# Kernel optimization log

Measured on AMD Instinct MI355X. Metric: run time of the kernel, lower is better.

Reference implementation:

```python
import jax, jax.numpy as jnp
import numpy as np

L, N, I, H = 512, 64, 1024, 1024


def setup_inputs() -> dict:
    key = jax.random.key(0)
    ks = jax.random.split(key, 7)
    s = 0.05
    return {
        "x": jax.random.normal(ks[0], (L, N, I), dtype=jnp.float32),
        "h0": jnp.zeros((N, H), dtype=jnp.float32),
        "c0": jnp.zeros((N, H), dtype=jnp.float32),
        "W_ih": jax.random.normal(ks[1], (4 * H, I), dtype=jnp.float32) * s,
        "W_hh": jax.random.normal(ks[2], (4 * H, H), dtype=jnp.float32) * s,
        "b_ih": jax.random.normal(ks[3], (4 * H,), dtype=jnp.float32) * s,
        "b_hh": jax.random.normal(ks[4], (4 * H,), dtype=jnp.float32) * s,
        "W_out": jax.random.normal(ks[5], (I, H), dtype=jnp.float32) * s,
        "b_out": jax.random.normal(ks[6], (I,), dtype=jnp.float32) * s,
    }


def reference(x, h0, c0, W_ih, W_hh, b_ih, b_hh, W_out, b_out):
    # PyTorch LSTMCell gate order: input, forget, cell(g), output
    b = b_ih + b_hh  # fuse the two bias adds

    def step(carry, xt):
        h, c = carry
        z = xt @ W_ih.T + h @ W_hh.T + b  # [N, 4H]
        i, f, g, o = jnp.split(z, 4, axis=1)
        c = jax.nn.sigmoid(f) * c + jax.nn.sigmoid(i) * jnp.tanh(g)
        h = jax.nn.sigmoid(o) * jnp.tanh(c)
        return (h, c), None

    (h, c), _ = jax.lax.scan(step, (h0, c0), x)
    y = h @ W_out.T + b_out  # [N, I]
    return (y, h, c)
```

## Files before the change

### kernel.cpp

```cpp
#include <hip/hip_runtime.h>
#include <hip/hip_bf16.h>


#define L_STEPS 512
#define NB 64
#define HID 1024
#define GRID_LSTM 128

typedef __bf16 bf16x8 __attribute__((ext_vector_type(8)));
typedef __bf16 bf16x4 __attribute__((ext_vector_type(4)));
typedef __bf16 bf16x2 __attribute__((ext_vector_type(2)));
typedef float  f32x4  __attribute__((ext_vector_type(4)));
typedef float  f32x2  __attribute__((ext_vector_type(2)));
typedef unsigned u32x4 __attribute__((ext_vector_type(4)));

__device__ __forceinline__ float sigmoid_f(float x) {
    return 1.f / (1.f + __expf(-x));
}
__device__ __forceinline__ float tanh_f(float x) {
    return 1.f - 2.f / (1.f + __expf(2.f * x));
}

__global__ void convert_kernel(const float* __restrict__ x, const float* __restrict__ h0,
                               __bf16* __restrict__ xbf, __bf16* __restrict__ hbf,
                               unsigned* __restrict__ bar) {
    unsigned u = blockIdx.x * 256u + threadIdx.x;
    if (u < 512u) bar[u] = 0u;
    const int row = u & 63;
    const int cg  = (u >> 6) & 127;
    if (u < 8192u) {
        const float* s = h0 + (size_t)row * HID + cg * 8;
        f32x4 a = *(const f32x4*)s, b = *(const f32x4*)(s + 4);
        bf16x8 o;
        o[0]=(__bf16)a[0]; o[1]=(__bf16)a[1]; o[2]=(__bf16)a[2]; o[3]=(__bf16)a[3];
        o[4]=(__bf16)b[0]; o[5]=(__bf16)b[1]; o[6]=(__bf16)b[2]; o[7]=(__bf16)b[3];
        ((bf16x8*)hbf)[u] = o;
    }
    const int t = u >> 13;
    const float* s = x + ((size_t)t * NB + row) * HID + cg * 8;
    f32x4 a = *(const f32x4*)s, b = *(const f32x4*)(s + 4);
    bf16x8 o;
    o[0]=(__bf16)a[0]; o[1]=(__bf16)a[1]; o[2]=(__bf16)a[2]; o[3]=(__bf16)a[3];
    o[4]=(__bf16)b[0]; o[5]=(__bf16)b[1]; o[6]=(__bf16)b[2]; o[7]=(__bf16)b[3];
    ((bf16x8*)xbf)[u] = o;
}

__device__ __forceinline__ void mfma_x(const __bf16* __restrict__ act,
                                       const bf16x8 (&wfr)[2][8],
                                       f32x4 (&acc)[2][4]) {
    #pragma unroll
    for (int kk = 0; kk < 8; ++kk) {
        bf16x8 bfr[4];
        #pragma unroll
        for (int nt = 0; nt < 4; ++nt)
            bfr[nt] = *(const bf16x8*)(act + kk * 2048 + nt * 128);
        #pragma unroll
        for (int mt = 0; mt < 2; ++mt)
            #pragma unroll
            for (int nt = 0; nt < 4; ++nt)
                acc[mt][nt] = __builtin_amdgcn_mfma_f32_16x16x32_bf16(
                    wfr[mt][kk], bfr[nt], acc[mt][nt], 0, 0, 0);
    }
}

template <bool RING>
__global__ __launch_bounds__(256, 1) void lstm_kernel(
    const float* __restrict__ c0,
    const float* __restrict__ W_ih, const float* __restrict__ W_hh,
    const float* __restrict__ b_ih, const float* __restrict__ b_hh,
    const __bf16* __restrict__ xbf,
    __bf16* hbuf,
    unsigned* bar,
    float* __restrict__ out)
{
    const int tid  = threadIdx.x;
    const int lane = tid & 63;
    const int w    = tid >> 6;
    const int quad = lane >> 4;
    const int l15  = lane & 15;
    const int hbase = blockIdx.x * 8;

    __shared__ float red[4][64][44];

    bf16x8 wfx[2][8], wfh[2][8];
    #pragma unroll
    for (int mt = 0; mt < 2; ++mt) {
        const int n    = mt * 16 + l15;
        const int grow = (n >> 3) * HID + hbase + (n & 7);
        #pragma unroll
        for (int kk = 0; kk < 8; ++kk) {
            const int kcol = w * 256 + kk * 32 + quad * 8;
            {
                const float* src = W_ih + (size_t)grow * 1024 + kcol;
                f32x4 a = *(const f32x4*)src;
                f32x4 b = *(const f32x4*)(src + 4);
                bf16x8 f;
                f[0]=(__bf16)a[0]; f[1]=(__bf16)a[1]; f[2]=(__bf16)a[2]; f[3]=(__bf16)a[3];
                f[4]=(__bf16)b[0]; f[5]=(__bf16)b[1]; f[6]=(__bf16)b[2]; f[7]=(__bf16)b[3];
                wfx[mt][kk] = f;
            }
            {
                const float* src = W_hh + (size_t)grow * 1024 + kcol;
                f32x4 a = *(const f32x4*)src;
                f32x4 b = *(const f32x4*)(src + 4);
                bf16x8 f;
                f[0]=(__bf16)a[0]; f[1]=(__bf16)a[1]; f[2]=(__bf16)a[2]; f[3]=(__bf16)a[3];
                f[4]=(__bf16)b[0]; f[5]=(__bf16)b[1]; f[6]=(__bf16)b[2]; f[7]=(__bf16)b[3];
                wfh[mt][kk] = f;
            }
        }
    }

    const int p0 = tid * 2;
    const int cb = p0 >> 3;
    const int cu = p0 & 7;
    float c0v = c0[cb * HID + hbase + cu];
    float c1v = c0[cb * HID + hbase + cu + 1];

    float bias0[4], bias1[4];
    #pragma unroll
    for (int gate = 0; gate < 4; ++gate) {
        int gr = gate * HID + hbase + cu;
        bias0[gate] = b_ih[gr] + b_hh[gr];
        bias1[gate] = b_ih[gr + 1] + b_hh[gr + 1];
    }

    const int lane_off = (32 * w + quad) * 512 + l15 * 8;
    const int hstore_off = blockIdx.x * 512 + cb * 8 + cu;

    f32x4 acc[2][4];
    #pragma unroll
    for (int mt = 0; mt < 2; ++mt)
        #pragma unroll
        for (int nt = 0; nt < 4; ++nt) { f32x4 z = {0.f,0.f,0.f,0.f}; acc[mt][nt] = z; }
    mfma_x(xbf + lane_off, wfx, acc);

    const int pf0 = 128 * w + lane;
    const int pf1 = 128 * w + 64 + lane;

    for (int t = 0; t < L_STEPS; ++t) {
        for (;;) {
            unsigned f0 = __hip_atomic_load(&bar[pf0], __ATOMIC_RELAXED,
                                            __HIP_MEMORY_SCOPE_AGENT);
            unsigned f1 = __hip_atomic_load(&bar[pf1], __ATOMIC_RELAXED,
                                            __HIP_MEMORY_SCOPE_AGENT);
            if (__all((f0 >= (unsigned)t) && (f1 >= (unsigned)t))) break;
            __builtin_amdgcn_s_sleep(1);
        }

        u32x4 hb[8][4];
        const __bf16* hb_base = hbuf
            + (size_t)(RING ? t : (t & 1)) * (NB * HID) + lane_off;
        #pragma unroll
        for (int kk = 0; kk < 8; ++kk)
            #pragma unroll
            for (int nt = 0; nt < 4; ++nt) {
                const __bf16* p = hb_base + kk * 2048 + nt * 128;
                if constexpr (RING)
                    asm volatile("global_load_dwordx4 %0, %1, off"
                                 : "=v"(hb[kk][nt]) : "v"(p));
                else
                    asm volatile("global_load_dwordx4 %0, %1, off sc1"
                                 : "=v"(hb[kk][nt]) : "v"(p));
            }
        asm volatile("s_waitcnt vmcnt(16)"
            : "+v"(hb[0][0]), "+v"(hb[0][1]), "+v"(hb[0][2]), "+v"(hb[0][3]),
              "+v"(hb[1][0]), "+v"(hb[1][1]), "+v"(hb[1][2]), "+v"(hb[1][3]),
              "+v"(hb[2][0]), "+v"(hb[2][1]), "+v"(hb[2][2]), "+v"(hb[2][3]),
              "+v"(hb[3][0]), "+v"(hb[3][1]), "+v"(hb[3][2]), "+v"(hb[3][3]));
        #pragma unroll
        for (int kk = 0; kk < 4; ++kk)
            #pragma unroll
            for (int mt = 0; mt < 2; ++mt)
                #pragma unroll
                for (int nt = 0; nt < 4; ++nt)
                    acc[mt][nt] = __builtin_amdgcn_mfma_f32_16x16x32_bf16(
                        wfh[mt][kk], __builtin_bit_cast(bf16x8, hb[kk][nt]),
                        acc[mt][nt], 0, 0, 0);
        asm volatile("s_waitcnt vmcnt(0)"
            : "+v"(hb[4][0]), "+v"(hb[4][1]), "+v"(hb[4][2]), "+v"(hb[4][3]),
              "+v"(hb[5][0]), "+v"(hb[5][1]), "+v"(hb[5][2]), "+v"(hb[5][3]),
              "+v"(hb[6][0]), "+v"(hb[6][1]), "+v"(hb[6][2]), "+v"(hb[6][3]),
              "+v"(hb[7][0]), "+v"(hb[7][1]), "+v"(hb[7][2]), "+v"(hb[7][3]));
        #pragma unroll
        for (int kk = 4; kk < 8; ++kk)
            #pragma unroll
            for (int mt = 0; mt < 2; ++mt)
                #pragma unroll
                for (int nt = 0; nt < 4; ++nt)
                    acc[mt][nt] = __builtin_amdgcn_mfma_f32_16x16x32_bf16(
                        wfh[mt][kk], __builtin_bit_cast(bf16x8, hb[kk][nt]),
                        acc[mt][nt], 0, 0, 0);

        __syncthreads();

        #pragma unroll
        for (int mt = 0; mt < 2; ++mt)
            #pragma unroll
            for (int nt = 0; nt < 4; ++nt) {
                const int row0 = mt * 16 + quad * 4;
                const int col  = nt * 16 + l15;
                *(f32x4*)&red[w][col][row0] = acc[mt][nt];
            }
        __syncthreads();

        float h0v, h1v;
        {
            float z0[4], z1[4];
            #pragma unroll
            for (int gate = 0; gate < 4; ++gate) {
                const int row = gate * 8 + cu;
                f32x2 s0 = *(const f32x2*)&red[0][cb][row];
                f32x2 s1 = *(const f32x2*)&red[1][cb][row];
                f32x2 s2 = *(const f32x2*)&red[2][cb][row];
                f32x2 s3 = *(const f32x2*)&red[3][cb][row];
                z0[gate] = s0[0] + s1[0] + s2[0] + s3[0] + bias0[gate];
                z1[gate] = s0[1] + s1[1] + s2[1] + s3[1] + bias1[gate];
            }
            float ig = sigmoid_f(z0[0]), fg = sigmoid_f(z0[1]);
            float gg = tanh_f(z0[2]),    og = sigmoid_f(z0[3]);
            c0v = fg * c0v + ig * gg;
            h0v = og * tanh_f(c0v);
            ig = sigmoid_f(z1[0]); fg = sigmoid_f(z1[1]);
            gg = tanh_f(z1[2]);    og = sigmoid_f(z1[3]);
            c1v = fg * c1v + ig * gg;
            h1v = og * tanh_f(c1v);
        }

        {
            bf16x2 hv; hv[0] = (__bf16)h0v; hv[1] = (__bf16)h1v;
            unsigned hbits = __builtin_bit_cast(unsigned, hv);
            const __bf16* dst = hbuf
                + (size_t)(RING ? (t + 1) : ((t + 1) & 1)) * (NB * HID) + hstore_off;
            asm volatile("global_store_dword %0, %1, off sc1"
                         :: "v"(dst), "v"(hbits) : "memory");
        }
        if (t == L_STEPS - 1) {
            const int idx = cb * HID + hbase + cu;
            out[65536 + idx]      = h0v;
            out[65536 + idx + 1]  = h1v;
            out[131072 + idx]     = c0v;
            out[131072 + idx + 1] = c1v;
        }
        asm volatile("s_waitcnt vmcnt(0)" ::: "memory");
        if (lane == 0)
            __hip_atomic_store(&bar[blockIdx.x * 4 + w], (unsigned)(t + 1),
                               __ATOMIC_RELAXED, __HIP_MEMORY_SCOPE_AGENT);

        #pragma unroll
        for (int mt = 0; mt < 2; ++mt)
            #pragma unroll
            for (int nt = 0; nt < 4; ++nt) { f32x4 z = {0.f,0.f,0.f,0.f}; acc[mt][nt] = z; }
        if (t < L_STEPS - 1)
            mfma_x(xbf + (size_t)(t + 1) * (NB * HID) + lane_off, wfx, acc);
    }
}

__global__ void out_kernel(const float* __restrict__ base, const float* __restrict__ Wout,
                           const float* __restrict__ bout, float* __restrict__ y)
{
    const int wv   = (int)((blockIdx.x * 256u + threadIdx.x) >> 6);
    const int lane = threadIdx.x & 63;
    const int b = wv >> 10;
    const int i = wv & 1023;
    const f32x4* hp = (const f32x4*)(base + 65536 + b * HID);
    const f32x4* wp = (const f32x4*)(Wout + (size_t)i * HID);
    float acc = 0.f;
    #pragma unroll
    for (int q = 0; q < 4; ++q) {
        f32x4 hv = hp[q * 64 + lane];
        f32x4 wvv = wp[q * 64 + lane];
        acc += hv[0]*wvv[0] + hv[1]*wvv[1] + hv[2]*wvv[2] + hv[3]*wvv[3];
    }
    #pragma unroll
    for (int off = 32; off > 0; off >>= 1) acc += __shfl_down(acc, off);
    if (lane == 0) y[b * HID + i] = acc + bout[i];
}

extern "C" void kernel_launch(void* const* d_in, const int* in_sizes, int n_in,
                              void* d_out, int out_size, void* d_ws, size_t ws_size,
                              hipStream_t stream)
{
    const float* x    = (const float*)d_in[0];
    const float* h0   = (const float*)d_in[1];
    const float* c0   = (const float*)d_in[2];
    const float* W_ih = (const float*)d_in[3];
    const float* W_hh = (const float*)d_in[4];
    const float* b_ih = (const float*)d_in[5];
    const float* b_hh = (const float*)d_in[6];
    const float* Wout = (const float*)d_in[7];
    const float* bout = (const float*)d_in[8];
    float* out = (float*)d_out;

    const size_t XBF_B  = 67108864;
    const size_t RING_B = 513ull * 131072;
    const size_t need_ring = XBF_B + RING_B + 2048;
    const bool ring = ws_size >= need_ring;

    char* ws = (char*)d_ws;
    __bf16* xbf   = (__bf16*)(ws);
    __bf16* hbuf  = (__bf16*)(ws + XBF_B);
    unsigned* bar = (unsigned*)(ws + XBF_B + (ring ? RING_B : 262144));

    convert_kernel<<<16384, 256, 0, stream>>>(x, h0, xbf, hbuf, bar);
    if (ring)
        lstm_kernel<true><<<GRID_LSTM, 256, 0, stream>>>(c0, W_ih, W_hh, b_ih, b_hh,
                                                         xbf, hbuf, bar, out);
    else
        lstm_kernel<false><<<GRID_LSTM, 256, 0, stream>>>(c0, W_ih, W_hh, b_ih, b_hh,
                                                          xbf, hbuf, bar, out);
    out_kernel<<<16384, 256, 0, stream>>>(out, Wout, bout, out);
}
```

Baseline: 2.918 ms.

## Replace flag barrier with poison-value polling on ring buffer hidden state

In ring mode, the per-wave flag barrier is removed. Every ring slot after the first is prefilled with a poison bit pattern during conversion, and consumers read h directly, reloading any chunk that still contains the poison value. This removes the flag store, the vmcnt drain before it and the separate flag polling from the per-step critical path. The trade-off is a correctness risk: a legitimate bf16 pair equal to the poison pattern would spin forever. The prefill also adds extra write traffic in the convert kernel.

```diff
diff --git a/kernel.cpp b/kernel.cpp
--- a/kernel.cpp
+++ b/kernel.cpp
@@ -6,6 +6,7 @@
 #define NB 64
 #define HID 1024
 #define GRID_LSTM 128
+#define PZN 0xAAAAAAAAu
 
 typedef __bf16 bf16x8 __attribute__((ext_vector_type(8)));
 typedef __bf16 bf16x4 __attribute__((ext_vector_type(4)));
@@ -23,7 +24,7 @@
 
 __global__ void convert_kernel(const float* __restrict__ x, const float* __restrict__ h0,
                                __bf16* __restrict__ xbf, __bf16* __restrict__ hbf,
-                               unsigned* __restrict__ bar) {
+                               unsigned* __restrict__ bar, int ring) {
     unsigned u = blockIdx.x * 256u + threadIdx.x;
     if (u < 512u) bar[u] = 0u;
     const int row = u & 63;
@@ -36,6 +37,10 @@
         o[4]=(__bf16)b[0]; o[5]=(__bf16)b[1]; o[6]=(__bf16)b[2]; o[7]=(__bf16)b[3];
         ((bf16x8*)hbf)[u] = o;
     }
+    if (ring) {
+        u32x4 P = {PZN, PZN, PZN, PZN};
+        ((u32x4*)(hbf + NB * HID))[u] = P;
+    }
     const int t = u >> 13;
     const float* s = x + ((size_t)t * NB + row) * HID + cg * 8;
     f32x4 a = *(const f32x4*)s, b = *(const f32x4*)(s + 4);
@@ -62,6 +67,41 @@
                     wfr[mt][kk], bfr[nt], acc[mt][nt], 0, 0, 0);
     }
 }
+
+template <int K0>
+__device__ __forceinline__ unsigned pmask16(const u32x4 (&hb)[8][4]) {
+    unsigned bad = 0u;
+    #pragma unroll
+    for (int kk = K0; kk < K0 + 4; ++kk)
+        #pragma unroll
+        for (int nt = 0; nt < 4; ++nt) {
+            const u32x4 v = hb[kk][nt];
+            bad |= (unsigned)(v[0] == PZN);
+            bad |= (unsigned)(v[1] == PZN);
+            bad |= (unsigned)(v[2] == PZN);
+            bad |= (unsigned)(v[3] == PZN);
+        }
+    return bad;
+}
+
+template <int K0>
+__device__ __forceinline__ void reload16(u32x4 (&hb)[8][4], const __bf16* hb_base) {
+    #pragma unroll
+    for (int kk = K0; kk < K0 + 4; ++kk)
+        #pragma unroll
+        for (int nt = 0; nt < 4; ++nt) {
+            const __bf16* p = hb_base + kk * 2048 + nt * 128;
+            asm volatile("global_load_dwordx4 %0, %1, off sc0 sc1"
+                         : "=v"(hb[kk][nt]) : "v"(p));
+        }
+}
+
+#define WAITDEP16(N, B)                                                        \
+    asm volatile("s_waitcnt vmcnt(" #N ")"                                     \
+        : "+v"(hb[B+0][0]), "+v"(hb[B+0][1]), "+v"(hb[B+0][2]), "+v"(hb[B+0][3]),\
+          "+v"(hb[B+1][0]), "+v"(hb[B+1][1]), "+v"(hb[B+1][2]), "+v"(hb[B+1][3]),\
+          "+v"(hb[B+2][0]), "+v"(hb[B+2][1]), "+v"(hb[B+2][2]), "+v"(hb[B+2][3]),\
+          "+v"(hb[B+3][0]), "+v"(hb[B+3][1]), "+v"(hb[B+3][2]), "+v"(hb[B+3][3]))
 
 template <bool RING>
 __global__ __launch_bounds__(256, 1) void lstm_kernel(
@@ -139,13 +179,15 @@
     const int pf1 = 128 * w + 64 + lane;
 
     for (int t = 0; t < L_STEPS; ++t) {
-        for (;;) {
-            unsigned f0 = __hip_atomic_load(&bar[pf0], __ATOMIC_RELAXED,
-                                            __HIP_MEMORY_SCOPE_AGENT);
-            unsigned f1 = __hip_atomic_load(&bar[pf1], __ATOMIC_RELAXED,
-                                            __HIP_MEMORY_SCOPE_AGENT);
-            if (__all((f0 >= (unsigned)t) && (f1 >= (unsigned)t))) break;
-            __builtin_amdgcn_s_sleep(1);
+        if constexpr (!RING) {
+            for (;;) {
+                unsigned f0 = __hip_atomic_load(&bar[pf0], __ATOMIC_RELAXED,
+                                                __HIP_MEMORY_SCOPE_AGENT);
+                unsigned f1 = __hip_atomic_load(&bar[pf1], __ATOMIC_RELAXED,
+                                                __HIP_MEMORY_SCOPE_AGENT);
+                if (__all((f0 >= (unsigned)t) && (f1 >= (unsigned)t))) break;
+                __builtin_amdgcn_s_sleep(1);
+            }
         }
 
         u32x4 hb[8][4];
@@ -163,11 +205,16 @@
                     asm volatile("global_load_dwordx4 %0, %1, off sc1"
                                  : "=v"(hb[kk][nt]) : "v"(p));
             }
-        asm volatile("s_waitcnt vmcnt(16)"
-            : "+v"(hb[0][0]), "+v"(hb[0][1]), "+v"(hb[0][2]), "+v"(hb[0][3]),
-              "+v"(hb[1][0]), "+v"(hb[1][1]), "+v"(hb[1][2]), "+v"(hb[1][3]),
-              "+v"(hb[2][0]), "+v"(hb[2][1]), "+v"(hb[2][2]), "+v"(hb[2][3]),
-              "+v"(hb[3][0]), "+v"(hb[3][1]), "+v"(hb[3][2]), "+v"(hb[3][3]));
+        WAITDEP16(16, 0);
+        if constexpr (RING) {
+            unsigned bad = pmask16<0>(hb);
+            while (__any((int)bad)) {
+                __builtin_amdgcn_s_sleep(1);
+                reload16<0>(hb, hb_base);
+                WAITDEP16(0, 0);
+                bad = pmask16<0>(hb);
+            }
+        }
         #pragma unroll
         for (int kk = 0; kk < 4; ++kk)
             #pragma unroll
@@ -177,11 +224,16 @@
                     acc[mt][nt] = __builtin_amdgcn_mfma_f32_16x16x32_bf16(
                         wfh[mt][kk], __builtin_bit_cast(bf16x8, hb[kk][nt]),
                         acc[mt][nt], 0, 0, 0);
-        asm volatile("s_waitcnt vmcnt(0)"
-            : "+v"(hb[4][0]), "+v"(hb[4][1]), "+v"(hb[4][2]), "+v"(hb[4][3]),
-              "+v"(hb[5][0]), "+v"(hb[5][1]), "+v"(hb[5][2]), "+v"(hb[5][3]),
-              "+v"(hb[6][0]), "+v"(hb[6][1]), "+v"(hb[6][2]), "+v"(hb[6][3]),
-              "+v"(hb[7][0]), "+v"(hb[7][1]), "+v"(hb[7][2]), "+v"(hb[7][3]));
+        WAITDEP16(0, 4);
+        if constexpr (RING) {
+            unsigned bad = pmask16<4>(hb);
+            while (__any((int)bad)) {
+                __builtin_amdgcn_s_sleep(1);
+                reload16<4>(hb, hb_base);
+                WAITDEP16(0, 4);
+                bad = pmask16<4>(hb);
+            }
+        }
         #pragma unroll
         for (int kk = 4; kk < 8; ++kk)
             #pragma unroll
@@ -242,10 +294,12 @@
             out[131072 + idx]     = c0v;
             out[131072 + idx + 1] = c1v;
         }
-        asm volatile("s_waitcnt vmcnt(0)" ::: "memory");
-        if (lane == 0)
-            __hip_atomic_store(&bar[blockIdx.x * 4 + w], (unsigned)(t + 1),
-                               __ATOMIC_RELAXED, __HIP_MEMORY_SCOPE_AGENT);
+        if constexpr (!RING) {
+            asm volatile("s_waitcnt vmcnt(0)" ::: "memory");
+            if (lane == 0)
+                __hip_atomic_store(&bar[blockIdx.x * 4 + w], (unsigned)(t + 1),
+                                   __ATOMIC_RELAXED, __HIP_MEMORY_SCOPE_AGENT);
+        }
 
         #pragma unroll
         for (int mt = 0; mt < 2; ++mt)
@@ -302,7 +356,7 @@
     __bf16* hbuf  = (__bf16*)(ws + XBF_B);
     unsigned* bar = (unsigned*)(ws + XBF_B + (ring ? RING_B : 262144));
 
-    convert_kernel<<<16384, 256, 0, stream>>>(x, h0, xbf, hbuf, bar);
+    convert_kernel<<<16384, 256, 0, stream>>>(x, h0, xbf, hbuf, bar, (int)ring);
     if (ring)
         lstm_kernel<true><<<GRID_LSTM, 256, 0, stream>>>(c0, W_ih, W_hh, b_ih, b_hh,
                                                          xbf, hbuf, bar, out);
```

Measured after the change: 3.218 ms. 1.1x slower.
